# Optimization experiments

Measured on AMD Instinct MI355X. Metric: run time of the kernel, lower is better.

The kernel has to match this reference:

```python
import jax, jax.numpy as jnp
import numpy as np

MARGIN = 5.0


def setup_inputs() -> dict:
    key = jax.random.key(0)
    k1, k2, k3 = jax.random.split(key, 3)
    B, D, C = 8192, 128, 100
    inputs = jax.random.normal(k1, (B, D), dtype=jnp.float32)
    targets = jax.random.randint(k2, (B,), 0, C, dtype=jnp.int64)
    centers = jax.random.normal(k3, (C, D), dtype=jnp.float32)
    return {"inputs": inputs, "targets": targets, "centers": centers}


def reference(inputs, targets, centers):
    # centers_batch[j] = centers[targets[j]]  -> [B, D]
    cb = centers[targets]
    # dist[i, j] = || inputs[i] - centers[targets[j]] ||  (clamped, sqrt)
    # computed via the GEMM expansion instead of a [B,B,D] diff tensor
    x2 = jnp.sum(inputs * inputs, axis=1)            # [B]
    c2 = jnp.sum(cb * cb, axis=1)                    # [B]
    d2 = x2[:, None] + c2[None, :] - 2.0 * (inputs @ cb.T)  # [B, B]
    dist = jnp.sqrt(jnp.clip(d2, 1e-12))
    # mask[i, j] = (targets[i] == targets[j])
    mask = targets[:, None] == targets[None, :]
    # hardest positive (max over same class), hardest negative (min over other classes)
    dist_ap = jnp.max(jnp.where(mask, dist, -jnp.inf), axis=1)  # [B]
    dist_an = jnp.min(jnp.where(mask, jnp.inf, dist), axis=1)   # [B]
    # MarginRankingLoss with y=1: mean(relu(margin + dist_ap - dist_an))
    return jnp.mean(jax.nn.relu(MARGIN + dist_ap - dist_an))
```

## Files before the change

### kernel.cpp

```cpp
#include <hip/hip_runtime.h>
#include <math.h>


constexpr int T = 256;
constexpr int RPB = 16;
constexpr int RPW = 4;
constexpr int CPAD = 112;
constexpr int C = 100;
constexpr float MARGIN = 5.0f;

constexpr int CEN_CHUNKS = CPAD * 32;
constexpr int LDS_X_OFF  = CEN_CHUNKS * 16;
constexpr int LDS_C2     = 65536;
constexpr int LDS_X2     = 66048;
constexpr int LDS_PRES   = 66112;
constexpr int LDS_WRED   = 66240;
constexpr int LDS_TOTAL  = 66304;

__device__ __forceinline__ float4 fma4(float4 a, float4 b, float4 c) {
    return make_float4(fmaf(a.x, b.x, c.x), fmaf(a.y, b.y, c.y),
                       fmaf(a.z, b.z, c.z), fmaf(a.w, b.w, c.w));
}
__device__ __forceinline__ float hsum4(float4 v) {
    return (v.x + v.y) + (v.z + v.w);
}

__global__ __launch_bounds__(256) void tcl_main(
    const float* __restrict__ x, const int* __restrict__ tgt,
    const float* __restrict__ cen, float* __restrict__ partial, int B)
{
    __shared__ __align__(16) char lds[LDS_TOTAL];
    float* c2s = (float*)(lds + LDS_C2);
    float* x2s = (float*)(lds + LDS_X2);
    unsigned char* present = (unsigned char*)(lds + LDS_PRES);
    float* wred = (float*)(lds + LDS_WRED);

    const int tid  = threadIdx.x;
    const int bid  = blockIdx.x;
    const int lane = tid & 63;
    const int wid  = __builtin_amdgcn_readfirstlane(tid >> 6);
    const float* xblk = x + (size_t)bid * RPB * 128;

    #pragma unroll
    for (int k = 0; k < 16; ++k) {
        const int j = k * T + tid;
        const char* src;
        if (k < 14) {
            const int cl  = j >> 5;
            const int scl = (cl < C) ? cl : 0;
            const int srcChunk = scl * 32 + ((j & 31) ^ ((scl >> 1) & 7));
            src = (const char*)cen + srcChunk * 16;
        } else {
            src = (const char*)xblk + (size_t)(j - CEN_CHUNKS) * 16;
        }
        __builtin_amdgcn_global_load_lds(
            (const __attribute__((address_space(1))) void*)src,
            (__attribute__((address_space(3))) void*)(lds + (size_t)(k * T + wid * 64) * 16),
            16, 0, 0);
    }

    if (wid == 2) {
        present[lane] = 0; present[64 + lane] = 0;
        for (int it = 0; it < 32; ++it) {
            const int4 tv = reinterpret_cast<const int4*>(tgt)[it * 64 + lane];
            present[tv.x] = 1; present[tv.y] = 1;
            present[tv.z] = 1; present[tv.w] = 1;
        }
    } else if (wid == 3) {
        float4 acc = make_float4(0.f, 0.f, 0.f, 0.f);
        #pragma unroll
        for (int c = 0; c < 8; ++c) {
            const float4 v = reinterpret_cast<const float4*>(xblk)[lane * 8 + c];
            acc = fma4(v, v, acc);
        }
        float s = hsum4(acc);
        s += __shfl_xor(s, 1);
        s += __shfl_xor(s, 2);
        if ((lane & 3) == 0) x2s[lane >> 2] = s;
    }
    __syncthreads();

    if (tid < 128) {
        float val = 0.f;
        if (tid < CPAD) {
            const int vbb = tid * 512 + (((tid >> 1) & 7) << 4);
            float4 acc = make_float4(0.f, 0.f, 0.f, 0.f);
            #pragma unroll 8
            for (int e = 0; e < 32; ++e) {
                const float4 v = *reinterpret_cast<const float4*>(lds + (vbb ^ (e << 4)));
                acc = fma4(v, v, acc);
            }
            val = hsum4(acc);
        }
        c2s[tid] = val;
    }
    __syncthreads();

    const char* xld = lds + LDS_X_OFF + wid * RPW * 512;
    const int vb = lane * 1024 + ((lane & 7) << 4);

    float4 a[RPW][2];
    #pragma unroll
    for (int r = 0; r < RPW; ++r) {
        a[r][0] = make_float4(0.f, 0.f, 0.f, 0.f);
        a[r][1] = make_float4(0.f, 0.f, 0.f, 0.f);
    }

    #pragma unroll 4
    for (int d4 = 0; d4 < 32; ++d4) {
        float4 xv[RPW];
        #pragma unroll
        for (int r = 0; r < RPW; ++r)
            xv[r] = *reinterpret_cast<const float4*>(xld + r * 512 + d4 * 16);
        const char* p = lds + (vb ^ (d4 << 4));
        const float4 cv0 = *reinterpret_cast<const float4*>(p);
        const float4 cv1 = *reinterpret_cast<const float4*>(p + 512);
        #pragma unroll
        for (int r = 0; r < RPW; ++r) {
            a[r][0] = fma4(xv[r], cv0, a[r][0]);
            a[r][1] = fma4(xv[r], cv1, a[r][1]);
        }
    }

    const int rowg = bid * RPB + wid * RPW;
    int tr[RPW]; float x2v[RPW];
    #pragma unroll
    for (int r = 0; r < RPW; ++r) {
        tr[r]  = tgt[rowg + r];
        x2v[r] = x2s[wid * RPW + r];
    }
    const int cl0 = 2 * lane, cl1 = 2 * lane + 1;
    const float c20 = c2s[cl0], c21 = c2s[cl1];
    const bool p0 = present[cl0] != 0, p1 = present[cl1] != 0;

    float term = 0.f;
    #pragma unroll
    for (int r = 0; r < RPW; ++r) {
        const float d20 = fmaxf(x2v[r] + c20 - 2.f * hsum4(a[r][0]), 1e-12f);
        const float d21 = fmaxf(x2v[r] + c21 - 2.f * hsum4(a[r][1]), 1e-12f);
        float ap = (cl0 == tr[r]) ? d20 : ((cl1 == tr[r]) ? d21 : -1.f);
        float an = fminf((p0 && cl0 != tr[r]) ? d20 : INFINITY,
                         (p1 && cl1 != tr[r]) ? d21 : INFINITY);
        #pragma unroll
        for (int off = 1; off < 64; off <<= 1) {
            ap = fmaxf(ap, __shfl_xor(ap, off));
            an = fminf(an, __shfl_xor(an, off));
        }
        term += fmaxf(0.f, MARGIN + sqrtf(ap) - sqrtf(an));
    }

    if (lane == 0) wred[wid] = term;
    __syncthreads();
    if (tid == 0) partial[bid] = (wred[0] + wred[1]) + (wred[2] + wred[3]);
}

__global__ __launch_bounds__(256) void tcl_reduce(
    const float* __restrict__ partial, float* __restrict__ out, float invB)
{
    __shared__ float wred[4];
    const int tid = threadIdx.x;
    float v = partial[tid] + partial[tid + 256];
    #pragma unroll
    for (int off = 1; off < 64; off <<= 1) v += __shfl_xor(v, off);
    if ((tid & 63) == 0) wred[tid >> 6] = v;
    __syncthreads();
    if (tid == 0)
        out[0] = ((wred[0] + wred[1]) + (wred[2] + wred[3])) * invB;
}

extern "C" void kernel_launch(void* const* d_in, const int* in_sizes, int n_in,
                              void* d_out, int out_size, void* d_ws, size_t ws_size,
                              hipStream_t stream)
{
    const float* x   = (const float*)d_in[0];
    const int*   tgt = (const int*)d_in[1];
    const float* cen = (const float*)d_in[2];
    float* out = (float*)d_out;
    float* partial = (float*)d_ws;

    const int B = in_sizes[1];
    const int nblocks = B / RPB;

    tcl_main<<<nblocks, T, 0, stream>>>(x, tgt, cen, partial, B);
    tcl_reduce<<<1, 256, 0, stream>>>(partial, out, 1.0f / (float)B);
}
```

Baseline: 18.17 us.

## Double rows per block and fuse final reduction via cooperative grid sync

Each block now handles 32 rows (8 per wave) instead of 16, which halves the number of blocks to 256 and the number of times the centers table is reloaded into LDS. The separate reduction kernel is folded into a cooperative launch that uses a grid-wide sync, after which block 0 sums the partials. This removes one kernel launch but adds grid-barrier overhead, more registers for the doubled accumulators, and a larger LDS footprint per block. If the cooperative launch fails, the code falls back to the previous two-kernel path.

```diff
diff --git a/kernel.cpp b/kernel.cpp
--- a/kernel.cpp
+++ b/kernel.cpp
@@ -1,21 +1,26 @@
 #include <hip/hip_runtime.h>
+#include <hip/hip_cooperative_groups.h>
 #include <math.h>
 
+namespace cg = cooperative_groups;
+
 
 constexpr int T = 256;
-constexpr int RPB = 16;
-constexpr int RPW = 4;
+constexpr int RPB = 32;
+constexpr int RPW = 8;
 constexpr int CPAD = 112;
 constexpr int C = 100;
 constexpr float MARGIN = 5.0f;
 
 constexpr int CEN_CHUNKS = CPAD * 32;
+constexpr int X_CHUNKS   = RPB * 32;
+constexpr int ALL_CHUNKS = CEN_CHUNKS + X_CHUNKS;
 constexpr int LDS_X_OFF  = CEN_CHUNKS * 16;
-constexpr int LDS_C2     = 65536;
-constexpr int LDS_X2     = 66048;
-constexpr int LDS_PRES   = 66112;
-constexpr int LDS_WRED   = 66240;
-constexpr int LDS_TOTAL  = 66304;
+constexpr int LDS_C2     = 73728;
+constexpr int LDS_X2     = 74240;
+constexpr int LDS_PRES   = 74368;
+constexpr int LDS_WRED   = 74496;
+constexpr int LDS_TOTAL  = 74512;
 
 __device__ __forceinline__ float4 fma4(float4 a, float4 b, float4 c) {
     return make_float4(fmaf(a.x, b.x, c.x), fmaf(a.y, b.y, c.y),
@@ -25,11 +30,11 @@
     return (v.x + v.y) + (v.z + v.w);
 }
 
-__global__ __launch_bounds__(256) void tcl_main(
+__device__ __forceinline__ void tcl_body(
     const float* __restrict__ x, const int* __restrict__ tgt,
-    const float* __restrict__ cen, float* __restrict__ partial, int B)
-{
-    __shared__ __align__(16) char lds[LDS_TOTAL];
+    const float* __restrict__ cen, float* __restrict__ partial,
+    char* lds, int B)
+{
     float* c2s = (float*)(lds + LDS_C2);
     float* x2s = (float*)(lds + LDS_X2);
     unsigned char* present = (unsigned char*)(lds + LDS_PRES);
@@ -42,7 +47,7 @@
     const float* xblk = x + (size_t)bid * RPB * 128;
 
     #pragma unroll
-    for (int k = 0; k < 16; ++k) {
+    for (int k = 0; k < 18; ++k) {
         const int j = k * T + tid;
         const char* src;
         if (k < 14) {
@@ -67,16 +72,16 @@
             present[tv.z] = 1; present[tv.w] = 1;
         }
     } else if (wid == 3) {
+        const int row = lane >> 1, h = lane & 1;
         float4 acc = make_float4(0.f, 0.f, 0.f, 0.f);
         #pragma unroll
-        for (int c = 0; c < 8; ++c) {
-            const float4 v = reinterpret_cast<const float4*>(xblk)[lane * 8 + c];
+        for (int c = 0; c < 16; ++c) {
+            const float4 v = reinterpret_cast<const float4*>(xblk)[row * 32 + h * 16 + c];
             acc = fma4(v, v, acc);
         }
         float s = hsum4(acc);
         s += __shfl_xor(s, 1);
-        s += __shfl_xor(s, 2);
-        if ((lane & 3) == 0) x2s[lane >> 2] = s;
+        if (h == 0) x2s[row] = s;
     }
     __syncthreads();
 
@@ -154,12 +159,42 @@
     if (tid == 0) partial[bid] = (wred[0] + wred[1]) + (wred[2] + wred[3]);
 }
 
+__global__ __launch_bounds__(256) void tcl_coop(
+    const float* __restrict__ x, const int* __restrict__ tgt,
+    const float* __restrict__ cen, float* __restrict__ partial,
+    float* __restrict__ out, int B, float invB)
+{
+    __shared__ __align__(16) char lds[LDS_TOTAL];
+    tcl_body(x, tgt, cen, partial, lds, B);
+
+    cg::this_grid().sync();
+    if (blockIdx.x == 0) {
+        float* wred = (float*)(lds + LDS_WRED);
+        const int tid = threadIdx.x;
+        float v = partial[tid];
+        #pragma unroll
+        for (int off = 1; off < 64; off <<= 1) v += __shfl_xor(v, off);
+        if ((tid & 63) == 0) wred[tid >> 6] = v;
+        __syncthreads();
+        if (tid == 0)
+            out[0] = ((wred[0] + wred[1]) + (wred[2] + wred[3])) * invB;
+    }
+}
+
+__global__ __launch_bounds__(256) void tcl_main(
+    const float* __restrict__ x, const int* __restrict__ tgt,
+    const float* __restrict__ cen, float* __restrict__ partial, int B)
+{
+    __shared__ __align__(16) char lds[LDS_TOTAL];
+    tcl_body(x, tgt, cen, partial, lds, B);
+}
+
 __global__ __launch_bounds__(256) void tcl_reduce(
     const float* __restrict__ partial, float* __restrict__ out, float invB)
 {
     __shared__ float wred[4];
     const int tid = threadIdx.x;
-    float v = partial[tid] + partial[tid + 256];
+    float v = partial[tid];
     #pragma unroll
     for (int off = 1; off < 64; off <<= 1) v += __shfl_xor(v, off);
     if ((tid & 63) == 0) wred[tid >> 6] = v;
@@ -178,9 +213,16 @@
     float* out = (float*)d_out;
     float* partial = (float*)d_ws;
 
-    const int B = in_sizes[1];
+    int B = in_sizes[1];
+    float invB = 1.0f / (float)B;
     const int nblocks = B / RPB;
 
-    tcl_main<<<nblocks, T, 0, stream>>>(x, tgt, cen, partial, B);
-    tcl_reduce<<<1, 256, 0, stream>>>(partial, out, 1.0f / (float)B);
-}
+    void* args[] = { (void*)&x, (void*)&tgt, (void*)&cen,
+                     (void*)&partial, (void*)&out, (void*)&B, (void*)&invB };
+    hipError_t err = hipLaunchCooperativeKernel((void*)tcl_coop, dim3(nblocks),
+                                                dim3(T), args, 0, stream);
+    if (err != hipSuccess) {
+        tcl_main<<<nblocks, T, 0, stream>>>(x, tgt, cen, partial, B);
+        tcl_reduce<<<1, 256, 0, stream>>>(partial, out, invB);
+    }
+}
```

After: 54.69 us. 201% more time.
